# Kernel tuning notes

Hardware: AMD Instinct MI355X
Metric: run time of the kernel (lower is better)

Reference implementation:

```python
import jax, jax.numpy as jnp
import numpy as np

B, T, D_MODEL, NHEAD, D_HEAD = 8, 4096, 1024, 16, 64


def setup_inputs() -> dict:
    key = jax.random.key(0)
    ks = jax.random.split(key, 8)
    return {
        "inputs": jax.random.normal(ks[0], (B, T, D_MODEL), jnp.float32),
        "z0": jax.random.normal(ks[1], (NHEAD, D_HEAD), jnp.float32),
        "W_in": jax.random.normal(ks[2], (D_MODEL, D_MODEL), jnp.float32) / np.sqrt(D_MODEL),
        "b_in": jax.random.normal(ks[3], (D_MODEL,), jnp.float32) * 0.01,
        "W_out": jax.random.normal(ks[4], (D_MODEL, D_MODEL), jnp.float32) / np.sqrt(D_MODEL),
        "b_out": jax.random.normal(ks[5], (D_MODEL,), jnp.float32) * 0.01,
        "smoothing_logit": jax.random.normal(ks[6], (NHEAD, 1), jnp.float32),
        "v0": jax.random.normal(ks[7], (1, 1, NHEAD, D_HEAD), jnp.float32),
    }


def reference(inputs, z0, W_in, b_in, W_out, b_out, smoothing_logit, v0):
    b, t, d = inputs.shape
    nhead, d_head = z0.shape
    # in projection -> (b, t, h, d_head)
    values = (inputs @ W_in + b_in).reshape(b, t, nhead, d_head)
    # prepend learned z0, then temporal differencing -> (b, t, h, d_head)
    z0_b = jnp.broadcast_to(z0[None, None], (b, 1, nhead, d_head))
    values = jnp.concatenate([z0_b, values], axis=1)
    values = values[:, 1:] - values[:, :-1]
    # exponential smoothing recurrence: s_j = a*s_{j-1} + (1-a)*v_j, s_{-1} = v0
    alpha = jax.nn.sigmoid(smoothing_logit)           # (h, 1)
    a = alpha[None]                                   # (1, h, 1) broadcast over batch
    s0 = jnp.broadcast_to(v0[0, 0][None], (b, nhead, d_head))

    def step(s, v):                                   # v: (b, h, d_head)
        s = a * s + (1.0 - a) * v
        return s, s

    _, es_out = jax.lax.scan(step, s0, jnp.swapaxes(values, 0, 1))  # (t, b, h, d)
    es_out = jnp.swapaxes(es_out, 0, 1)               # (b, t, h, d_head)
    # prepend v0 -> length t+1
    v0_b = jnp.broadcast_to(v0, (b, 1, nhead, d_head))
    out = jnp.concatenate([v0_b, es_out], axis=1)     # (b, t+1, h, d_head)
    out = out.reshape(b, t + 1, nhead * d_head)
    return out @ W_out + b_out                        # (b, t+1, d_model)
```

## Files before the change

### kernel.cpp

```cpp
#include <hip/hip_runtime.h>
#include <hip/hip_bf16.h>
#include <stdint.h>

#define DEV static __device__ __forceinline__

typedef __attribute__((ext_vector_type(8))) short bf16x8;
typedef __attribute__((ext_vector_type(4))) float f32x4;
typedef unsigned int u32;

static constexpr int T = 4096;
static constexpr int BATCH = 8;
static constexpr int DM = 1024;
static constexpr int M1 = BATCH * T;
static constexpr int M2 = BATCH * (T + 1);
static constexpr int M2P = 129 * 256;
static constexpr int NCH = 64;
static constexpr int CL = T / NCH;
static constexpr int NT = 32;

DEV unsigned short f2bf(float f) {
  union { float f; unsigned u; } v; v.f = f;
  unsigned u = v.u;
  return (unsigned short)((u + 0x7fffu + ((u >> 16) & 1u)) >> 16);
}
DEV float bf2f(unsigned short s) {
  union { unsigned u; float f; } v; v.u = ((unsigned)s) << 16;
  return v.f;
}

DEV void gl_lds16(const unsigned short* g, unsigned short* lds) {
  __builtin_amdgcn_global_load_lds(
      (const __attribute__((address_space(1))) u32*)g,
      (__attribute__((address_space(3))) u32*)lds,
      16, 0, 0);
}

__global__ void k_cvt_x(const float4* __restrict__ x, ushort4* __restrict__ o) {
  int i = blockIdx.x * 256 + threadIdx.x;
  float4 v = x[i];
  ushort4 r;
  r.x = f2bf(v.x); r.y = f2bf(v.y); r.z = f2bf(v.z); r.w = f2bf(v.w);
  o[i] = r;
}

__global__ void k_transpose(const float* __restrict__ w0, const float* __restrict__ w1,
                            unsigned short* __restrict__ t0, unsigned short* __restrict__ t1) {
  __shared__ float tile[32][33];
  const float* src = blockIdx.z ? w1 : w0;
  unsigned short* dst = blockIdx.z ? t1 : t0;
  int bx = blockIdx.x * 32;
  int by = blockIdx.y * 32;
  int tx = threadIdx.x & 31, ty = threadIdx.x >> 5;
#pragma unroll
  for (int r = 0; r < 32; r += 8)
    tile[ty + r][tx] = src[(by + ty + r) * DM + bx + tx];
  __syncthreads();
#pragma unroll
  for (int r = 0; r < 32; r += 8)
    dst[(bx + ty + r) * DM + by + tx] = f2bf(tile[tx][ty + r]);
}

template <int MODE>
__global__ __launch_bounds__(512, 4) void k_gemm(const unsigned short* __restrict__ A16,
                                                 const unsigned short* __restrict__ Bt16,
                                                 const float* __restrict__ bias,
                                                 unsigned short* __restrict__ outb,
                                                 float* __restrict__ outf, int Mvalid) {
  __shared__ unsigned short lds[24576];

  const int tid = threadIdx.x;
  const int w = tid >> 6, l = tid & 63;
  const int wm = w >> 1, wn = w & 1;
  const int lo = l & 15, hi = l >> 4;

  const int nwg = gridDim.x, orig = blockIdx.x;
  const int cpx = nwg >> 3;
  const int wg = (orig & 7) * cpx + (orig >> 3);
  const int bm = wg >> 3, bn = wg & 7;
  const int blockM = bm * 256;
  const int blockN = bn * 128;

  f32x4 acc[4][4];
#pragma unroll
  for (int m = 0; m < 4; m++)
#pragma unroll
    for (int n = 0; n < 4; n++) acc[m][n] = (f32x4){0.f, 0.f, 0.f, 0.f};

  const int sg = (l & 3) ^ ((l >> 3) & 3);
  const unsigned short* pA[2];
#pragma unroll
  for (int c = 0; c < 2; c++)
    pA[c] = A16 + (size_t)(blockM + w * 32 + c * 16 + (l >> 2)) * DM + sg * 8;
  const unsigned short* pB =
      Bt16 + (size_t)(blockN + w * 16 + (l >> 2)) * DM + sg * 8;

  auto stage = [&](int tt, int buf) {
#pragma unroll
    for (int c = 0; c < 2; c++)
      gl_lds16(pA[c] + (size_t)tt * 32, &lds[buf * 12288 + (w * 32 + c * 16) * 32]);
    gl_lds16(pB + (size_t)tt * 32, &lds[buf * 12288 + 8192 + (w * 16) * 32]);
  };

  stage(0, 0);
  __syncthreads();

  for (int t = 0; t < NT; ++t) {
    const int cur = t & 1;
    if (t + 1 < NT) stage(t + 1, cur ^ 1);

    bf16x8 aq[4], bq[4];
#pragma unroll
    for (int mf = 0; mf < 4; mf++) {
      const int r = wm * 64 + mf * 16 + lo;
      aq[mf] = *(const bf16x8*)(&lds[cur * 12288 + r * 32 + (hi ^ ((r >> 1) & 3)) * 8]);
    }
#pragma unroll
    for (int nf = 0; nf < 4; nf++) {
      const int r = wn * 64 + nf * 16 + lo;
      bq[nf] = *(const bf16x8*)(&lds[cur * 12288 + 8192 + r * 32 + (hi ^ ((r >> 1) & 3)) * 8]);
    }
#pragma unroll
    for (int mf = 0; mf < 4; mf++)
#pragma unroll
      for (int nf = 0; nf < 4; nf++)
        acc[mf][nf] = __builtin_amdgcn_mfma_f32_16x16x32_bf16(
            bq[nf], aq[mf], acc[mf][nf], 0, 0, 0);

    __syncthreads();
  }

#pragma unroll
  for (int mf = 0; mf < 4; mf++) {
    const int row = blockM + wm * 64 + mf * 16 + lo;
    if (MODE == 1 && row >= Mvalid) continue;
#pragma unroll
    for (int nf = 0; nf < 4; nf++) {
      const int col = blockN + wn * 64 + nf * 16 + hi * 4;
      const float4 bv = *(const float4*)(bias + col);
      if (MODE == 0) {
        ushort4 o;
        o.x = f2bf(acc[mf][nf][0] + bv.x);
        o.y = f2bf(acc[mf][nf][1] + bv.y);
        o.z = f2bf(acc[mf][nf][2] + bv.z);
        o.w = f2bf(acc[mf][nf][3] + bv.w);
        *(ushort4*)(outb + (size_t)row * DM + col) = o;
      } else {
        float4 o;
        o.x = acc[mf][nf][0] + bv.x;
        o.y = acc[mf][nf][1] + bv.y;
        o.z = acc[mf][nf][2] + bv.z;
        o.w = acc[mf][nf][3] + bv.w;
        *(float4*)(outf + (size_t)row * DM + col) = o;
      }
    }
  }
}

__global__ void k_scan_partial(const unsigned short* __restrict__ proj,
                               const float* __restrict__ logit,
                               const float* __restrict__ z0,
                               float* __restrict__ chunkend) {
  const int b = blockIdx.x >> 6, c = blockIdx.x & 63;
  const int ch0 = threadIdx.x * 8;
  const float a = 1.f / (1.f + expf(-logit[ch0 >> 6]));
  const int t0 = c * CL;
  const unsigned short* p = proj + (size_t)(b * T + t0) * DM + ch0;
  float pprev[8], s[8];
  if (t0 == 0) {
#pragma unroll
    for (int k = 0; k < 8; k++) pprev[k] = z0[ch0 + k];
  } else {
    bf16x8 v = *(const bf16x8*)(p - DM);
#pragma unroll
    for (int k = 0; k < 8; k++) pprev[k] = bf2f((unsigned short)v[k]);
  }
#pragma unroll
  for (int k = 0; k < 8; k++) s[k] = 0.f;
  for (int j = 0; j < CL; j++) {
    bf16x8 v = *(const bf16x8*)(p + (size_t)j * DM);
#pragma unroll
    for (int k = 0; k < 8; k++) {
      float pv = bf2f((unsigned short)v[k]);
      s[k] = a * s[k] + (1.f - a) * (pv - pprev[k]);
      pprev[k] = pv;
    }
  }
  float* o = chunkend + (size_t)(b * NCH + c) * DM + ch0;
#pragma unroll
  for (int k = 0; k < 4; k++) ((float2*)o)[k] = make_float2(s[2 * k], s[2 * k + 1]);
}

__global__ void k_scan_combine(const float* __restrict__ chunkend,
                               const float* __restrict__ logit,
                               const float* __restrict__ v0,
                               float* __restrict__ enter) {
  const int b = blockIdx.x;
  const int ch0 = threadIdx.x * 4;
  const float a = 1.f / (1.f + expf(-logit[ch0 >> 6]));
  const float a2 = a * a, a4 = a2 * a2, a8 = a4 * a4, a16 = a8 * a8, a32 = a16 * a16;
  const float aL = a32 * a32;
  float4 e = *(const float4*)(v0 + ch0);
  *(float4*)(enter + (size_t)(b * NCH) * DM + ch0) = e;
  for (int c = 1; c < NCH; c++) {
    const float4 ce = *(const float4*)(chunkend + (size_t)(b * NCH + c - 1) * DM + ch0);
    e.x = aL * e.x + ce.x;
    e.y = aL * e.y + ce.y;
    e.z = aL * e.z + ce.z;
    e.w = aL * e.w + ce.w;
    *(float4*)(enter + (size_t)(b * NCH + c) * DM + ch0) = e;
  }
}

__global__ void k_scan_final(const unsigned short* __restrict__ proj,
                             const float* __restrict__ logit,
                             const float* __restrict__ z0,
                             const float* __restrict__ v0,
                             const float* __restrict__ enter,
                             unsigned short* __restrict__ S) {
  const int b = blockIdx.x >> 6, c = blockIdx.x & 63;
  const int ch0 = threadIdx.x * 8;
  const float a = 1.f / (1.f + expf(-logit[ch0 >> 6]));
  const int t0 = c * CL;
  const unsigned short* p = proj + (size_t)(b * T + t0) * DM + ch0;
  unsigned short* so = S + (size_t)(b * (T + 1) + t0 + 1) * DM + ch0;
  float pprev[8], s[8];
  if (t0 == 0) {
#pragma unroll
    for (int k = 0; k < 8; k++) pprev[k] = z0[ch0 + k];
  } else {
    bf16x8 v = *(const bf16x8*)(p - DM);
#pragma unroll
    for (int k = 0; k < 8; k++) pprev[k] = bf2f((unsigned short)v[k]);
  }
  {
    const float* e = enter + (size_t)(b * NCH + c) * DM + ch0;
#pragma unroll
    for (int k = 0; k < 8; k++) s[k] = e[k];
  }
  if (c == 0) {
    bf16x8 r;
#pragma unroll
    for (int k = 0; k < 8; k++) r[k] = (short)f2bf(v0[ch0 + k]);
    *(bf16x8*)(S + (size_t)b * (T + 1) * DM + ch0) = r;
  }
  for (int j = 0; j < CL; j++) {
    bf16x8 v = *(const bf16x8*)(p + (size_t)j * DM);
    bf16x8 r;
#pragma unroll
    for (int k = 0; k < 8; k++) {
      float pv = bf2f((unsigned short)v[k]);
      s[k] = a * s[k] + (1.f - a) * (pv - pprev[k]);
      pprev[k] = pv;
      r[k] = (short)f2bf(s[k]);
    }
    *(bf16x8*)(so + (size_t)j * DM) = r;
  }
}

extern "C" void kernel_launch(void* const* d_in, const int* in_sizes, int n_in,
                              void* d_out, int out_size, void* d_ws, size_t ws_size,
                              hipStream_t stream) {
  const float* inputs = (const float*)d_in[0];
  const float* z0     = (const float*)d_in[1];
  const float* W_in   = (const float*)d_in[2];
  const float* b_in   = (const float*)d_in[3];
  const float* W_out  = (const float*)d_in[4];
  const float* b_out  = (const float*)d_in[5];
  const float* slogit = (const float*)d_in[6];
  const float* v0     = (const float*)d_in[7];
  float* out = (float*)d_out;

  char* ws = (char*)d_ws;
  unsigned short* X16   = (unsigned short*)(ws);
  unsigned short* P16   = (unsigned short*)(ws + 67108864);
  unsigned short* S16   = (unsigned short*)(ws + 134217728);
  unsigned short* WTin  = (unsigned short*)(ws + 201850880);
  unsigned short* WTout = (unsigned short*)(ws + 203948032);
  float* chunkend       = (float*)(ws + 206045184);
  float* enter          = (float*)(ws + 208142336);

  k_cvt_x<<<32768, 256, 0, stream>>>((const float4*)inputs, (ushort4*)X16);
  k_transpose<<<dim3(32, 32, 2), 256, 0, stream>>>(W_in, W_out, WTin, WTout);
  k_gemm<0><<<dim3((M1 / 256) * 8), 512, 0, stream>>>(X16, WTin, b_in, P16, nullptr, M1);
  k_scan_partial<<<dim3(BATCH * NCH), 128, 0, stream>>>(P16, slogit, z0, chunkend);
  k_scan_combine<<<dim3(BATCH), 256, 0, stream>>>(chunkend, slogit, v0, enter);
  k_scan_final<<<dim3(BATCH * NCH), 128, 0, stream>>>(P16, slogit, z0, v0, enter, S16);
  k_gemm<1><<<dim3((M2P / 256) * 8), 512, 0, stream>>>(S16, WTout, b_out, nullptr, out, M2);
}
```

Before: 278.0 us.

## Fuse chunk-partial scan sums into the input-projection GEMM epilogue

After: 279.5 us. About the same (+0.6%).

```diff
diff --git a/kernel.cpp b/kernel.cpp
--- a/kernel.cpp
+++ b/kernel.cpp
@@ -1,6 +1,7 @@
 #include <hip/hip_runtime.h>
 #include <hip/hip_bf16.h>
 #include <stdint.h>
+#include <math.h>
 
 #define DEV static __device__ __forceinline__
 
@@ -65,7 +66,10 @@
                                                  const unsigned short* __restrict__ Bt16,
                                                  const float* __restrict__ bias,
                                                  unsigned short* __restrict__ outb,
-                                                 float* __restrict__ outf, int Mvalid) {
+                                                 float* __restrict__ outf, int Mvalid,
+                                                 const float* __restrict__ slog,
+                                                 float* __restrict__ chunkL,
+                                                 float* __restrict__ plastg) {
   __shared__ unsigned short lds[24576];
 
   const int tid = threadIdx.x;
@@ -154,44 +158,66 @@
       }
     }
   }
-}
-
-__global__ void k_scan_partial(const unsigned short* __restrict__ proj,
+
+  if (MODE == 0) {
+    const float aa = 1.f / (1.f + expf(-slog[(blockN + wn * 64) >> 6]));
+    const float one_a = 1.f - aa;
+    const float a2v = aa * aa, a4v = a2v * a2v, a8v = a4v * a4v, a16v = a8v * a8v;
+    const float w3raw = powf(aa, (float)(14 - lo));
+    float wv[4];
+    wv[3] = (lo == 15) ? 0.f : w3raw;
+    wv[2] = w3raw * a16v;
+    wv[1] = wv[2] * a16v;
+    wv[0] = wv[1] * a16v;
+    float S[4][4], P63[4][4];
+#pragma unroll
+    for (int nf = 0; nf < 4; nf++) {
+      const int col = blockN + wn * 64 + nf * 16 + hi * 4;
+      const float4 bv = *(const float4*)(bias + col);
+#pragma unroll
+      for (int j = 0; j < 4; j++) {
+        const float bj = ((const float*)&bv)[j];
+        float s = 0.f, p63 = 0.f;
+#pragma unroll
+        for (int mf = 0; mf < 4; mf++) {
+          const float p = acc[mf][nf][j] + bj;
+          s += wv[mf] * p;
+          if (mf == 3 && lo == 15) p63 = p;
+        }
+        S[nf][j] = s;
+        P63[nf][j] = p63;
+      }
+    }
+#pragma unroll
+    for (int nf = 0; nf < 4; nf++)
+#pragma unroll
+      for (int j = 0; j < 4; j++)
+#pragma unroll
+        for (int m = 1; m < 16; m <<= 1) {
+          S[nf][j] += __shfl_xor(S[nf][j], m);
+          P63[nf][j] += __shfl_xor(P63[nf][j], m);
+        }
+    const int cglob = (blockM >> 6) + wm;
+    if (lo == 0 || lo == 1) {
+#pragma unroll
+      for (int nf = 0; nf < 4; nf++)
+#pragma unroll
+        for (int j = 0; j < 4; j++) {
+          const int col = blockN + wn * 64 + nf * 16 + hi * 4 + j;
+          if (lo == 0)
+            chunkL[(size_t)cglob * DM + col] =
+                one_a * P63[nf][j] - one_a * one_a * S[nf][j];
+          else
+            plastg[(size_t)cglob * DM + col] = P63[nf][j];
+        }
+    }
+  }
+}
+
+__global__ void k_scan_combine(const float* __restrict__ chunkL,
+                               const float* __restrict__ plastg,
                                const float* __restrict__ logit,
                                const float* __restrict__ z0,
-                               float* __restrict__ chunkend) {
-  const int b = blockIdx.x >> 6, c = blockIdx.x & 63;
-  const int ch0 = threadIdx.x * 8;
-  const float a = 1.f / (1.f + expf(-logit[ch0 >> 6]));
-  const int t0 = c * CL;
-  const unsigned short* p = proj + (size_t)(b * T + t0) * DM + ch0;
-  float pprev[8], s[8];
-  if (t0 == 0) {
-#pragma unroll
-    for (int k = 0; k < 8; k++) pprev[k] = z0[ch0 + k];
-  } else {
-    bf16x8 v = *(const bf16x8*)(p - DM);
-#pragma unroll
-    for (int k = 0; k < 8; k++) pprev[k] = bf2f((unsigned short)v[k]);
-  }
-#pragma unroll
-  for (int k = 0; k < 8; k++) s[k] = 0.f;
-  for (int j = 0; j < CL; j++) {
-    bf16x8 v = *(const bf16x8*)(p + (size_t)j * DM);
-#pragma unroll
-    for (int k = 0; k < 8; k++) {
-      float pv = bf2f((unsigned short)v[k]);
-      s[k] = a * s[k] + (1.f - a) * (pv - pprev[k]);
-      pprev[k] = pv;
-    }
-  }
-  float* o = chunkend + (size_t)(b * NCH + c) * DM + ch0;
-#pragma unroll
-  for (int k = 0; k < 4; k++) ((float2*)o)[k] = make_float2(s[2 * k], s[2 * k + 1]);
-}
-
-__global__ void k_scan_combine(const float* __restrict__ chunkend,
-                               const float* __restrict__ logit,
                                const float* __restrict__ v0,
                                float* __restrict__ enter) {
   const int b = blockIdx.x;
@@ -199,15 +225,18 @@
   const float a = 1.f / (1.f + expf(-logit[ch0 >> 6]));
   const float a2 = a * a, a4 = a2 * a2, a8 = a4 * a4, a16 = a8 * a8, a32 = a16 * a16;
   const float aL = a32 * a32;
+  const float g = (1.f - a) * a32 * a16 * a8 * a4 * a2 * a;
   float4 e = *(const float4*)(v0 + ch0);
+  float4 pp = *(const float4*)(z0 + ch0);
   *(float4*)(enter + (size_t)(b * NCH) * DM + ch0) = e;
   for (int c = 1; c < NCH; c++) {
-    const float4 ce = *(const float4*)(chunkend + (size_t)(b * NCH + c - 1) * DM + ch0);
-    e.x = aL * e.x + ce.x;
-    e.y = aL * e.y + ce.y;
-    e.z = aL * e.z + ce.z;
-    e.w = aL * e.w + ce.w;
+    const float4 L = *(const float4*)(chunkL + (size_t)(b * NCH + c - 1) * DM + ch0);
+    e.x = aL * e.x + (L.x - g * pp.x);
+    e.y = aL * e.y + (L.y - g * pp.y);
+    e.z = aL * e.z + (L.z - g * pp.z);
+    e.w = aL * e.w + (L.w - g * pp.w);
     *(float4*)(enter + (size_t)(b * NCH + c) * DM + ch0) = e;
+    pp = *(const float4*)(plastg + (size_t)(b * NCH + c - 1) * DM + ch0);
   }
 }
 
@@ -278,12 +307,14 @@
   unsigned short* WTout = (unsigned short*)(ws + 203948032);
   float* chunkend       = (float*)(ws + 206045184);
   float* enter          = (float*)(ws + 208142336);
+  float* plast          = (float*)(ws + 210239488);
 
   k_cvt_x<<<32768, 256, 0, stream>>>((const float4*)inputs, (ushort4*)X16);
   k_transpose<<<dim3(32, 32, 2), 256, 0, stream>>>(W_in, W_out, WTin, WTout);
-  k_gemm<0><<<dim3((M1 / 256) * 8), 512, 0, stream>>>(X16, WTin, b_in, P16, nullptr, M1);
-  k_scan_partial<<<dim3(BATCH * NCH), 128, 0, stream>>>(P16, slogit, z0, chunkend);
-  k_scan_combine<<<dim3(BATCH), 256, 0, stream>>>(chunkend, slogit, v0, enter);
+  k_gemm<0><<<dim3((M1 / 256) * 8), 512, 0, stream>>>(X16, WTin, b_in, P16, nullptr, M1,
+                                                      slogit, chunkend, plast);
+  k_scan_combine<<<dim3(BATCH), 256, 0, stream>>>(chunkend, plast, slogit, z0, v0, enter);
   k_scan_final<<<dim3(BATCH * NCH), 128, 0, stream>>>(P16, slogit, z0, v0, enter, S16);
-  k_gemm<1><<<dim3((M2P / 256) * 8), 512, 0, stream>>>(S16, WTout, b_out, nullptr, out, M2);
-}
+  k_gemm<1><<<dim3((M2P / 256) * 8), 512, 0, stream>>>(S16, WTout, b_out, nullptr, out, M2,
+                                                       nullptr, nullptr, nullptr);
+}
```

## Restructure bf16 GEMM to 256x256 tiles with K=64 stages and phased pipelining

Applied to the files above, without the earlier changes.

After: 299.6 us. 1.08x slower.

```diff
diff --git a/kernel.cpp b/kernel.cpp
--- a/kernel.cpp
+++ b/kernel.cpp
@@ -16,7 +16,7 @@
 static constexpr int M2P = 129 * 256;
 static constexpr int NCH = 64;
 static constexpr int CL = T / NCH;
-static constexpr int NT = 32;
+static constexpr int NT = 16;
 
 DEV unsigned short f2bf(float f) {
   union { float f; unsigned u; } v; v.f = f;
@@ -28,11 +28,17 @@
   return v.f;
 }
 
-DEV void gl_lds16(const unsigned short* g, unsigned short* lds) {
+DEV void gl_lds16(const unsigned short* g, void* lds) {
   __builtin_amdgcn_global_load_lds(
       (const __attribute__((address_space(1))) u32*)g,
       (__attribute__((address_space(3))) u32*)lds,
       16, 0, 0);
+}
+
+DEV bf16x8 ds_read128(unsigned byte_off) {
+  bf16x8 r;
+  asm volatile("ds_read_b128 %0, %1" : "=v"(r) : "v"(byte_off));
+  return r;
 }
 
 __global__ void k_cvt_x(const float4* __restrict__ x, ushort4* __restrict__ o) {
@@ -61,81 +67,116 @@
 }
 
 template <int MODE>
-__global__ __launch_bounds__(512, 4) void k_gemm(const unsigned short* __restrict__ A16,
+__global__ __launch_bounds__(512, 2) void k_gemm(const unsigned short* __restrict__ A16,
                                                  const unsigned short* __restrict__ Bt16,
                                                  const float* __restrict__ bias,
                                                  unsigned short* __restrict__ outb,
                                                  float* __restrict__ outf, int Mvalid) {
-  __shared__ unsigned short lds[24576];
+  __shared__ char smem[131072];
 
   const int tid = threadIdx.x;
   const int w = tid >> 6, l = tid & 63;
-  const int wm = w >> 1, wn = w & 1;
+  const int wm = w >> 2, wn = w & 3;
   const int lo = l & 15, hi = l >> 4;
 
   const int nwg = gridDim.x, orig = blockIdx.x;
-  const int cpx = nwg >> 3;
-  const int wg = (orig & 7) * cpx + (orig >> 3);
-  const int bm = wg >> 3, bn = wg & 7;
+  const int q8 = nwg >> 3, r8 = nwg & 7;
+  const int xcd = orig & 7, idx = orig >> 3;
+  const int wg = (xcd < r8 ? xcd * (q8 + 1) : r8 * (q8 + 1) + (xcd - r8) * q8) + idx;
+  const int bm = wg >> 2, bn = wg & 3;
   const int blockM = bm * 256;
-  const int blockN = bn * 128;
-
-  f32x4 acc[4][4];
-#pragma unroll
-  for (int m = 0; m < 4; m++)
+  const int blockN = bn * 256;
+
+  f32x4 acc[8][4];
+#pragma unroll
+  for (int m = 0; m < 8; m++)
 #pragma unroll
     for (int n = 0; n < 4; n++) acc[m][n] = (f32x4){0.f, 0.f, 0.f, 0.f};
 
-  const int sg = (l & 3) ^ ((l >> 3) & 3);
-  const unsigned short* pA[2];
-#pragma unroll
-  for (int c = 0; c < 2; c++)
-    pA[c] = A16 + (size_t)(blockM + w * 32 + c * 16 + (l >> 2)) * DM + sg * 8;
-  const unsigned short* pB =
-      Bt16 + (size_t)(blockN + w * 16 + (l >> 2)) * DM + sg * 8;
-
-  auto stage = [&](int tt, int buf) {
-#pragma unroll
-    for (int c = 0; c < 2; c++)
-      gl_lds16(pA[c] + (size_t)tt * 32, &lds[buf * 12288 + (w * 32 + c * 16) * 32]);
-    gl_lds16(pB + (size_t)tt * 32, &lds[buf * 12288 + 8192 + (w * 16) * 32]);
-  };
-
-  stage(0, 0);
-  __syncthreads();
-
-  for (int t = 0; t < NT; ++t) {
-    const int cur = t & 1;
-    if (t + 1 < NT) stage(t + 1, cur ^ 1);
-
-    bf16x8 aq[4], bq[4];
-#pragma unroll
-    for (int mf = 0; mf < 4; mf++) {
-      const int r = wm * 64 + mf * 16 + lo;
-      aq[mf] = *(const bf16x8*)(&lds[cur * 12288 + r * 32 + (hi ^ ((r >> 1) & 3)) * 8]);
-    }
+  const int srcs = (l & 7) ^ ((l >> 3) & 7);
+  const unsigned short* pG[2][2];
+#pragma unroll
+  for (int j = 0; j < 2; j++) {
+    const int rr = j * 64 + w * 8 + (l >> 3);
+    pG[0][j] = A16 + (size_t)(blockM + rr) * DM + srcs * 8;
+    pG[1][j] = Bt16 + (size_t)(blockN + rr) * DM + srcs * 8;
+  }
+
+#define STAGE(tt, OP, H)                                                        \
+  do {                                                                          \
+    char* d_ = smem + ((tt) & 1) * 65536 + (OP) * 32768 + (H) * 16384 + w * 1024; \
+    gl_lds16(pG[OP][0] + (size_t)(H) * 128 * DM + (size_t)(tt) * 64, d_);       \
+    gl_lds16(pG[OP][1] + (size_t)(H) * 128 * DM + (size_t)(tt) * 64, d_ + 8192); \
+  } while (0)
+
+  const unsigned ldsbase =
+      (unsigned)(size_t)(__attribute__((address_space(3))) char*)smem;
+  unsigned offA[4], offB[2], phy[2];
+#pragma unroll
+  for (int kh = 0; kh < 2; kh++) phy[kh] = (unsigned)(((kh * 4 + hi) ^ (lo & 7)) * 16);
+#pragma unroll
+  for (int mf = 0; mf < 4; mf++) offA[mf] = (unsigned)((mf * 32 + wm * 16 + lo) * 128);
+#pragma unroll
+  for (int nf = 0; nf < 2; nf++) offB[nf] = (unsigned)((nf * 64 + wn * 16 + lo) * 128);
+
+#define VM4 asm volatile("s_waitcnt vmcnt(4)" ::: "memory")
+#define VM0 asm volatile("s_waitcnt vmcnt(0)" ::: "memory")
+
+#define PH(SLOT, MH, NH, STG, WAIT)                                               \
+  do {                                                                           \
+    const unsigned bA_ = ldsbase + (SLOT) * 65536u + (MH) * 16384u;              \
+    const unsigned bB_ = ldsbase + (SLOT) * 65536u + 32768u + (NH) * 16384u;     \
+    bf16x8 aq_[4][2], bq_[2][2];                                                 \
+    _Pragma("unroll") for (int kh = 0; kh < 2; kh++) {                           \
+      _Pragma("unroll") for (int nf = 0; nf < 2; nf++)                           \
+        bq_[nf][kh] = ds_read128(bB_ + offB[nf] + phy[kh]);                      \
+      _Pragma("unroll") for (int mf = 0; mf < 4; mf++)                           \
+        aq_[mf][kh] = ds_read128(bA_ + offA[mf] + phy[kh]);                      \
+    }                                                                            \
+    STG;                                                                         \
+    WAIT;                                                                        \
+    __builtin_amdgcn_s_barrier();                                                \
+    asm volatile("s_waitcnt lgkmcnt(0)" ::: "memory");                           \
+    __builtin_amdgcn_sched_barrier(0);                                           \
+    __builtin_amdgcn_s_setprio(1);                                               \
+    _Pragma("unroll") for (int kh = 0; kh < 2; kh++)                             \
+      _Pragma("unroll") for (int mf = 0; mf < 4; mf++)                           \
+        _Pragma("unroll") for (int nf = 0; nf < 2; nf++)                         \
+          acc[(MH) * 4 + mf][(NH) * 2 + nf] =                                    \
+              __builtin_amdgcn_mfma_f32_16x16x32_bf16(                           \
+                  bq_[nf][kh], aq_[mf][kh], acc[(MH) * 4 + mf][(NH) * 2 + nf],   \
+                  0, 0, 0);                                                      \
+    __builtin_amdgcn_s_setprio(0);                                               \
+    __builtin_amdgcn_s_barrier();                                                \
+  } while (0)
+
+  STAGE(0, 0, 0); STAGE(0, 1, 0); STAGE(0, 0, 1); STAGE(0, 1, 1);
+  STAGE(1, 0, 0); STAGE(1, 1, 0);
+  VM4;
+  __builtin_amdgcn_s_barrier();
+
+  for (int i = 0; i < NT / 2; ++i) {
+    const int t1 = 2 * i + 1, t2 = 2 * i + 2, t3 = 2 * i + 3;
+    const bool g2 = (t2 < NT), g3 = (t3 < NT);
+    PH(0, 0, 0, STAGE(t1, 0, 1), );
+    PH(0, 0, 1, STAGE(t1, 1, 1), );
+    PH(0, 1, 0, if (g2) STAGE(t2, 0, 0), );
+    PH(0, 1, 1, if (g2) STAGE(t2, 1, 0), if (g2) { VM4; } else { VM0; });
+    PH(1, 0, 0, if (g2) STAGE(t2, 0, 1), );
+    PH(1, 0, 1, if (g2) STAGE(t2, 1, 1), );
+    PH(1, 1, 0, if (g3) STAGE(t3, 0, 0), );
+    PH(1, 1, 1, if (g3) STAGE(t3, 1, 0), if (g3) { VM4; } else { VM0; });
+  }
+#undef PH
+#undef STAGE
+
+#pragma unroll
+  for (int mf = 0; mf < 8; mf++) {
+    const int row = blockM + (mf >> 2) * 128 + (mf & 3) * 32 + wm * 16 + lo;
+    if (MODE == 1 && row >= Mvalid) continue;
 #pragma unroll
     for (int nf = 0; nf < 4; nf++) {
-      const int r = wn * 64 + nf * 16 + lo;
-      bq[nf] = *(const bf16x8*)(&lds[cur * 12288 + 8192 + r * 32 + (hi ^ ((r >> 1) & 3)) * 8]);
-    }
-#pragma unroll
-    for (int mf = 0; mf < 4; mf++)
-#pragma unroll
-      for (int nf = 0; nf < 4; nf++)
-        acc[mf][nf] = __builtin_amdgcn_mfma_f32_16x16x32_bf16(
-            bq[nf], aq[mf], acc[mf][nf], 0, 0, 0);
-
-    __syncthreads();
-  }
-
-#pragma unroll
-  for (int mf = 0; mf < 4; mf++) {
-    const int row = blockM + wm * 64 + mf * 16 + lo;
-    if (MODE == 1 && row >= Mvalid) continue;
-#pragma unroll
-    for (int nf = 0; nf < 4; nf++) {
-      const int col = blockN + wn * 64 + nf * 16 + hi * 4;
+      const int col = blockN + (nf >> 1) * 128 + (nf & 1) * 64 + wn * 16 + hi * 4;
       const float4 bv = *(const float4*)(bias + col);
       if (MODE == 0) {
         ushort4 o;
@@ -281,9 +322,9 @@
 
   k_cvt_x<<<32768, 256, 0, stream>>>((const float4*)inputs, (ushort4*)X16);
   k_transpose<<<dim3(32, 32, 2), 256, 0, stream>>>(W_in, W_out, WTin, WTout);
-  k_gemm<0><<<dim3((M1 / 256) * 8), 512, 0, stream>>>(X16, WTin, b_in, P16, nullptr, M1);
+  k_gemm<0><<<dim3((M1 / 256) * 4), 512, 0, stream>>>(X16, WTin, b_in, P16, nullptr, M1);
   k_scan_partial<<<dim3(BATCH * NCH), 128, 0, stream>>>(P16, slogit, z0, chunkend);
   k_scan_combine<<<dim3(BATCH), 256, 0, stream>>>(chunkend, slogit, v0, enter);
   k_scan_final<<<dim3(BATCH * NCH), 128, 0, stream>>>(P16, slogit, z0, v0, enter, S16);
-  k_gemm<1><<<dim3((M2P / 256) * 8), 512, 0, stream>>>(S16, WTout, b_out, nullptr, out, M2);
-}
+  k_gemm<1><<<dim3((M2P / 256) * 4), 512, 0, stream>>>(S16, WTout, b_out, nullptr, out, M2);
+}
```
